# Kernel tuning notes

Hardware: AMD Instinct MI355X
Metric: run time of the kernel (lower is better)

Reference implementation:

```python
import jax, jax.numpy as jnp
import numpy as np

NUM_LAYERS = 2
D_MODEL = 64
D_INNER = 128   # expand * d_model
D_STATE = 128   # min(2*input_size, 256)
DT_RANK = 4     # ceil(d_model / 16)
D_CONV = 4
HIDDEN = 64


def _causal_dwconv(x, w, b):
    # x: [B, L, C], w: [C, K], b: [C]  -- causal depthwise conv (left pad K-1)
    K = w.shape[1]
    L = x.shape[1]
    xp = jnp.pad(x, ((0, 0), (K - 1, 0), (0, 0)))
    y = sum(xp[:, k:k + L, :] * w[:, k][None, None, :] for k in range(K))
    return y + b


def _selective_scan(u, delta, A, B, C, Dp):
    # u, delta: [b,L,d]; A: [d,n]; B, C: [b,L,n]; Dp: [d]
    dA = jnp.exp(jnp.einsum('bld,dn->lbdn', delta, A))          # [L,b,d,n]
    dBu = jnp.einsum('bld,bln,bld->lbdn', delta, B, u)           # [L,b,d,n]
    Ct = jnp.swapaxes(C, 0, 1)                                   # [L,b,n]

    def step(h, inp):
        dA_t, dBu_t, C_t = inp
        h = dA_t * h + dBu_t                                     # [b,d,n]
        y = jnp.einsum('bdn,bn->bd', h, C_t)
        return h, y

    h0 = jnp.zeros(dA.shape[1:], dA.dtype)
    _, ys = jax.lax.scan(step, h0, (dA, dBu, Ct))                # ys: [L,b,d]
    return jnp.swapaxes(ys, 0, 1) + u * Dp


def _mamba_layer(x, in_w, conv_w, conv_b, xproj_w, dt_w, dt_b, A_log, Dp, out_w):
    xz = x @ in_w.T                                              # [B,L,2*d_inner]
    xi, z = jnp.split(xz, 2, axis=-1)
    xi = jax.nn.silu(_causal_dwconv(xi, conv_w, conv_b))
    xdbl = xi @ xproj_w.T                                        # [B,L,dt_rank+2*d_state]
    delta = jax.nn.softplus(xdbl[..., :DT_RANK] @ dt_w.T + dt_b)
    Bm = xdbl[..., DT_RANK:DT_RANK + D_STATE]
    Cm = xdbl[..., DT_RANK + D_STATE:]
    A = -jnp.exp(A_log)
    y = _selective_scan(xi, delta, A, Bm, Cm, Dp)
    y = y * jax.nn.silu(z)
    return y @ out_w.T


def setup_inputs() -> dict:
    key = jax.random.key(0)
    ks = jax.random.split(key, 10)
    B, L = 4, 1024
    s = 0.05
    x = jax.random.normal(ks[0], (B, L, D_MODEL), dtype=jnp.float32)
    in_proj_w = jax.random.normal(ks[1], (NUM_LAYERS, 2 * D_INNER, D_MODEL)) * s
    conv_w = jax.random.normal(ks[2], (NUM_LAYERS, D_INNER, D_CONV)) * 0.2
    conv_b = jax.random.normal(ks[3], (NUM_LAYERS, D_INNER)) * 0.02
    x_proj_w = jax.random.normal(ks[4], (NUM_LAYERS, DT_RANK + 2 * D_STATE, D_INNER)) * s
    dt_w = jax.random.normal(ks[5], (NUM_LAYERS, D_INNER, DT_RANK)) * 0.1
    dt_b = jnp.full((NUM_LAYERS, D_INNER), -4.6, dtype=jnp.float32)  # softplus -> ~0.01
    # S4D-real init: A_log = log(1..d_state)
    A_log = jnp.log(jnp.broadcast_to(
        jnp.arange(1, D_STATE + 1, dtype=jnp.float32), (NUM_LAYERS, D_INNER, D_STATE)))
    D = jnp.ones((NUM_LAYERS, D_INNER), dtype=jnp.float32)
    out_proj_w = jax.random.normal(ks[6], (NUM_LAYERS, D_MODEL, D_INNER)) * s
    fc_w = jax.random.normal(ks[7], (HIDDEN, D_MODEL)) * s
    fc_b = jax.random.normal(ks[8], (HIDDEN,)) * 0.02
    return {"x": x, "in_proj_w": in_proj_w, "conv_w": conv_w, "conv_b": conv_b,
            "x_proj_w": x_proj_w, "dt_w": dt_w, "dt_b": dt_b, "A_log": A_log,
            "D": D, "out_proj_w": out_proj_w, "fc_w": fc_w, "fc_b": fc_b}


def reference(x, in_proj_w, conv_w, conv_b, x_proj_w, dt_w, dt_b, A_log, D, out_proj_w, fc_w, fc_b):
    h = x
    for l in range(NUM_LAYERS):
        h = _mamba_layer(h, in_proj_w[l], conv_w[l], conv_b[l], x_proj_w[l],
                         dt_w[l], dt_b[l], A_log[l], D[l], out_proj_w[l])
    return h @ fc_w.T + fc_b
```

## Files before the change

### kernel.cpp

```cpp
#include <hip/hip_runtime.h>
#include <hip/hip_bf16.h>

#define BB 4
#define LL 1024
#define DM 64
#define DI 128
#define DS 128
#define DTR 4
#define KC 4
#define RT 8
#define SGRP 8
#define L2E 1.44269504f

#define XWT_OFF   0
#define INWT_OFF  65536
#define OWT_OFF   98304
#define CWT_OFF   114688
#define CB_OFF    115712
#define DTWT_OFF  115968
#define DTB_OFF   116992
#define XWDT_OFF  117248

__device__ __forceinline__ float silu_f(float x) { return x / (1.f + __expf(-x)); }

__device__ __forceinline__ float ldf(const void* p, long i, unsigned bf) {
    return bf ? __bfloat162float(((const __hip_bfloat16*)p)[i]) : ((const float*)p)[i];
}

__device__ __forceinline__ void fma4(float4& acc, float s, const float4 w) {
    acc.x = fmaf(s, w.x, acc.x); acc.y = fmaf(s, w.y, acc.y);
    acc.z = fmaf(s, w.z, acc.z); acc.w = fmaf(s, w.w, acc.w);
}

__device__ __forceinline__ void probe_flags(const void* dtb, const void* fcw,
                                            unsigned& bfe, unsigned& bfw) {
    unsigned w = *(const unsigned*)dtb;
    bfe = (w == 0xC093C093u) ? 1u : 0u;
    const unsigned* p = (const unsigned*)fcw;
    int cnt = 0;
    for (int i = 0; i < 32; ++i) {
        unsigned m = p[i] & 0x7FFFu;
        if (m >= 0x3000u && m < 0x4200u) cnt++;
    }
    bfw = (cnt >= 28) ? 1u : 0u;
}

__global__ __launch_bounds__(256) void k_prep(
        const void* __restrict__ inw, const void* __restrict__ xw,
        const void* __restrict__ ow, const void* __restrict__ cw,
        const void* __restrict__ cb, const void* __restrict__ dtw,
        const void* __restrict__ dtb, const void* __restrict__ fcw,
        unsigned* __restrict__ flags, float* __restrict__ WT) {
    unsigned bfe, bfw;
    probe_flags(dtb, fcw, bfe, bfw);
    int bid = blockIdx.x, tid = threadIdx.x;
    if (bid < 28) {
        const void* src; long soff; int srcK; float* dst; int dstN; int n0, k0;
        if (bid < 16) {
            int l = bid >> 3, kt = (bid >> 2) & 1, nt = bid & 3;
            src = xw; srcK = 128; soff = (long)l * 260 * 128 + 4 * 128;
            n0 = nt * 64; k0 = kt * 64; dst = WT + XWT_OFF + l * 32768; dstN = 256;
        } else if (bid < 24) {
            int b2 = bid - 16, l = b2 >> 2, nt = b2 & 3;
            src = inw; srcK = 64; soff = (long)l * 256 * 64;
            n0 = nt * 64; k0 = 0; dst = WT + INWT_OFF + l * 16384; dstN = 256;
        } else {
            int b2 = bid - 24, l = b2 >> 1, kt = b2 & 1;
            src = ow; srcK = 128; soff = (long)l * 64 * 128;
            n0 = 0; k0 = kt * 64; dst = WT + OWT_OFF + l * 8192; dstN = 64;
        }
        __shared__ float tile[64 * 65];
        for (int i = tid; i < 4096; i += 256) {
            int ln = i >> 6, lk = i & 63;
            tile[ln * 65 + lk] = ldf(src, soff + (long)(n0 + ln) * srcK + k0 + lk, bfw);
        }
        __syncthreads();
        for (int i = tid; i < 4096; i += 256) {
            int lk = i >> 6, ln = i & 63;
            dst[(long)(k0 + lk) * dstN + n0 + ln] = tile[ln * 65 + lk];
        }
    } else {
        if (tid == 0) { flags[0] = bfe; flags[1] = bfw; flags[2] = bfe & bfw; }
        for (int j = tid; j < 1024; j += 256) {
            int l = j >> 9, t = (j >> 7) & 3, d = j & 127;
            WT[CWT_OFF + j] = ldf(cw, (long)l * 512 + d * 4 + t, bfw);
        }
        for (int j = tid; j < 256; j += 256) WT[CB_OFF + j] = ldf(cb, j, bfw);
        for (int j = tid; j < 1024; j += 256) {
            int l = j >> 9, r = (j >> 7) & 3, d = j & 127;
            WT[DTWT_OFF + j] = ldf(dtw, (long)l * 512 + d * 4 + r, bfw);
        }
        for (int j = tid; j < 256; j += 256) WT[DTB_OFF + j] = ldf(dtb, j, bfe);
        for (int j = tid; j < 1024; j += 256) {
            int l = j >> 9, rem = j & 511;
            WT[XWDT_OFF + j] = ldf(xw, (long)l * 260 * 128 + rem, bfw);
        }
    }
}

__global__ __launch_bounds__(256) void k_inproj(
        const void* __restrict__ xin, int xin_probe,
        const float* __restrict__ wt, const unsigned* __restrict__ flags,
        float* __restrict__ xzx, float* __restrict__ sz) {
    unsigned bfx = xin_probe ? flags[0] : 0u;
    int row0 = blockIdx.x * RT;
    int tid = threadIdx.x, lane = tid & 63, g = tid >> 6;
    __shared__ float act[RT * DM];
    for (int i = tid; i < RT * DM; i += 256)
        act[i] = ldf(xin, (long)(row0 + (i >> 6)) * DM + (i & 63), bfx);
    __syncthreads();
    const float4* wt4 = (const float4*)wt;
    float4 acc[2];
    acc[0] = make_float4(0.f, 0.f, 0.f, 0.f);
    acc[1] = make_float4(0.f, 0.f, 0.f, 0.f);
#pragma unroll 8
    for (int k4 = 0; k4 < DM / 4; ++k4) {
        float4 w0 = wt4[(k4 * 4 + 0) * 64 + lane];
        float4 w1 = wt4[(k4 * 4 + 1) * 64 + lane];
        float4 w2 = wt4[(k4 * 4 + 2) * 64 + lane];
        float4 w3 = wt4[(k4 * 4 + 3) * 64 + lane];
#pragma unroll
        for (int r = 0; r < 2; ++r) {
            float4 av = *(const float4*)&act[(g * 2 + r) * DM + k4 * 4];
            fma4(acc[r], av.x, w0); fma4(acc[r], av.y, w1);
            fma4(acc[r], av.z, w2); fma4(acc[r], av.w, w3);
        }
    }
    int n0 = lane * 4;
#pragma unroll
    for (int r = 0; r < 2; ++r) {
        int row = row0 + g * 2 + r;
        if (n0 < DI) {
            *(float4*)&xzx[(size_t)row * DI + n0] = acc[r];
        } else {
            float4 v;
            v.x = silu_f(acc[r].x); v.y = silu_f(acc[r].y);
            v.z = silu_f(acc[r].z); v.w = silu_f(acc[r].w);
            *(float4*)&sz[(size_t)row * DI + (n0 - DI)] = v;
        }
    }
}

__global__ __launch_bounds__(256) void k_xproj(
        const float* __restrict__ xzx,
        const float* __restrict__ cwT, const float* __restrict__ cbF,
        const float* __restrict__ xwT, const float* __restrict__ xwdtF,
        const float* __restrict__ dtwT, const float* __restrict__ dtbF,
        float* __restrict__ xiw, float* __restrict__ dlt,
        float* __restrict__ Bm, float* __restrict__ Cm) {
    int row0 = blockIdx.x * RT;
    int b = row0 >> 10, l0 = row0 & (LL - 1);
    int tid = threadIdx.x, lane = tid & 63, g = tid >> 6;
    __shared__ float xc[(RT + KC - 1) * DI];
    __shared__ float act[RT * DI];
    __shared__ float dtp[RT * DTR];
    for (int i = tid; i < (RT + KC - 1) * DI; i += 256) {
        int r = (i >> 7) - (KC - 1);
        int l = l0 + r;
        xc[i] = (l >= 0) ? xzx[((size_t)b * LL + l) * DI + (i & 127)] : 0.f;
    }
    __syncthreads();
    for (int i = tid; i < RT * DI; i += 256) {
        int r = i >> 7, d = i & 127;
        float a = cbF[d];
#pragma unroll
        for (int t = 0; t < KC; ++t) a = fmaf(xc[(r + t) * DI + d], cwT[t * DI + d], a);
        float v = silu_f(a);
        act[i] = v;
        xiw[(size_t)(row0 + r) * DI + d] = v;
    }
    __syncthreads();
    const float4* wt4 = (const float4*)xwT;
    float4 acc[2];
    acc[0] = make_float4(0.f, 0.f, 0.f, 0.f);
    acc[1] = make_float4(0.f, 0.f, 0.f, 0.f);
#pragma unroll 8
    for (int k4 = 0; k4 < DI / 4; ++k4) {
        float4 w0 = wt4[(k4 * 4 + 0) * 64 + lane];
        float4 w1 = wt4[(k4 * 4 + 1) * 64 + lane];
        float4 w2 = wt4[(k4 * 4 + 2) * 64 + lane];
        float4 w3 = wt4[(k4 * 4 + 3) * 64 + lane];
#pragma unroll
        for (int r = 0; r < 2; ++r) {
            float4 av = *(const float4*)&act[(g * 2 + r) * DI + k4 * 4];
            fma4(acc[r], av.x, w0); fma4(acc[r], av.y, w1);
            fma4(acc[r], av.z, w2); fma4(acc[r], av.w, w3);
        }
    }
    int n0 = lane * 4;
#pragma unroll
    for (int r = 0; r < 2; ++r) {
        int row = row0 + g * 2 + r;
        if (n0 < DS) *(float4*)&Bm[(size_t)row * DS + n0] = acc[r];
        else         *(float4*)&Cm[(size_t)row * DS + (n0 - DS)] = acc[r];
    }
    if (tid < RT * DTR) {
        int r = tid >> 2, i = tid & 3;
        float a = 0.f;
#pragma unroll
        for (int k4 = 0; k4 < DI / 4; ++k4) {
            float4 av = *(const float4*)&act[r * DI + k4 * 4];
            float4 wv = *(const float4*)&xwdtF[i * DI + k4 * 4];
            a = fmaf(av.x, wv.x, a); a = fmaf(av.y, wv.y, a);
            a = fmaf(av.z, wv.z, a); a = fmaf(av.w, wv.w, a);
        }
        dtp[tid] = a;
    }
    __syncthreads();
    if (tid < DI) {
        float dw0 = dtwT[0 * DI + tid], dw1 = dtwT[1 * DI + tid];
        float dw2 = dtwT[2 * DI + tid], dw3 = dtwT[3 * DI + tid];
        float bv = dtbF[tid];
#pragma unroll
        for (int r = 0; r < RT; ++r) {
            float a = bv;
            a = fmaf(dtp[r * 4 + 0], dw0, a);
            a = fmaf(dtp[r * 4 + 1], dw1, a);
            a = fmaf(dtp[r * 4 + 2], dw2, a);
            a = fmaf(dtp[r * 4 + 3], dw3, a);
            dlt[(size_t)(row0 + r) * DI + tid] = (a > 20.f) ? a : log1pf(__expf(a));
        }
    }
}

#define SCAN_GROUP(LI, BV, CV)                                              \
    {                                                                       \
        float dl0[SGRP], du0[SGRP], ea[SGRP], cv[SGRP];                     \
        _Pragma("unroll") for (int s = 0; s < SGRP; ++s) {                  \
            dl0[s] = dsh[d_loc][(LI) + s];                                  \
            du0[s] = dush[d_loc][(LI) + s];                                 \
        }                                                                   \
        _Pragma("unroll") for (int s = 0; s < SGRP; ++s)                    \
            ea[s] = exp2f(dl0[s] * A);                                      \
        _Pragma("unroll") for (int s = 0; s < SGRP; ++s) {                  \
            h = fmaf(ea[s], h, du0[s] * BV[s]);                             \
            cv[s] = h * CV[s];                                              \
        }                                                                   \
        _Pragma("unroll") for (int s = 0; s < SGRP; ++s)                    \
            Wl[s * 65 + t] = cv[s];                                         \
        float pt = 0.f;                                                     \
        _Pragma("unroll") for (int j = 0; j < 8; ++j) pt += Wl[rbase + j];  \
        pt += __shfl_xor(pt, 1, 64);                                        \
        pt += __shfl_xor(pt, 2, 64);                                        \
        pt += __shfl_xor(pt, 4, 64);                                        \
        if ((t & 7) == 0) ysh[((LI) + (t >> 3)) * 4 + w] = pt;              \
    }

__global__ __launch_bounds__(256) void k_scan(
        const float* __restrict__ dlt, const float* __restrict__ xiw,
        const float* __restrict__ Bm, const float* __restrict__ Cm,
        const void* __restrict__ Alog, long aoff,
        const unsigned* __restrict__ flags,
        float* __restrict__ y) {
    __shared__ float dsh[2][LL];
    __shared__ float dush[2][LL];
    __shared__ float ysh[LL * 4];
    __shared__ float Wred[4 * 520];
    int bid = blockIdx.x;
    int b = bid >> 6, dg = bid & 63;
    int tid = threadIdx.x, w = tid >> 6, t = tid & 63;
    int d_loc = w >> 1, half = w & 1;
    int d = dg * 2 + d_loc;
    int n = half * 64 + t;
    unsigned bfe = flags[0];
    float A = -L2E * __expf(ldf(Alog, aoff + (long)d * DS + n, bfe));
    for (int i = tid; i < 2 * LL; i += 256) {
        int l = i >> 1, dd = i & 1;
        size_t src = ((size_t)b * LL + l) * DI + dg * 2 + dd;
        float dl = dlt[src];
        dsh[dd][l] = dl;
        dush[dd][l] = dl * xiw[src];
    }
    __syncthreads();
    const float* Bg = Bm + (size_t)b * LL * DS + n;
    const float* Cg = Cm + (size_t)b * LL * DS + n;
    float* Wl = Wred + w * 520;
    int rbase = (t >> 3) * 65 + (t & 7) * 8;
    float h = 0.f;
    float B0[SGRP], C0[SGRP], B1[SGRP], C1[SGRP];
#pragma unroll
    for (int s = 0; s < SGRP; ++s) {
        B0[s] = Bg[(size_t)s * DS];
        C0[s] = Cg[(size_t)s * DS];
    }
    for (int li = 0; li < LL; li += 2 * SGRP) {
#pragma unroll
        for (int s = 0; s < SGRP; ++s) {
            B1[s] = Bg[(size_t)(li + SGRP + s) * DS];
            C1[s] = Cg[(size_t)(li + SGRP + s) * DS];
        }
        SCAN_GROUP(li, B0, C0);
#pragma unroll
        for (int s = 0; s < SGRP; ++s) {
            B0[s] = Bg[(size_t)(li + 2 * SGRP + s) * DS];
            C0[s] = Cg[(size_t)(li + 2 * SGRP + s) * DS];
        }
        SCAN_GROUP(li + SGRP, B1, C1);
    }
    __syncthreads();
    for (int i = tid; i < LL * 2; i += 256) {
        int l = i >> 1, dd = i & 1;
        y[((size_t)b * LL + l) * DI + dg * 2 + dd] =
            ysh[l * 4 + dd * 2] + ysh[l * 4 + dd * 2 + 1];
    }
}

__global__ __launch_bounds__(256) void k_out(
        const float* __restrict__ y, const float* __restrict__ sz,
        const float* __restrict__ xiw,
        const void* __restrict__ Dp, long doff,
        const unsigned* __restrict__ flags,
        const float* __restrict__ owT, float* __restrict__ hout) {
    unsigned bfe = flags[0];
    int row0 = blockIdx.x * RT;
    int tid = threadIdx.x, n = tid & 63, g = tid >> 6;
    __shared__ float act[RT * DI];
    __shared__ float Dsh[DI];
    if (tid < DI) Dsh[tid] = ldf(Dp, doff + tid, bfe);
    __syncthreads();
    for (int i = tid; i < RT * DI; i += 256) {
        size_t idx = (size_t)(row0 + (i >> 7)) * DI + (i & 127);
        act[i] = (y[idx] + xiw[idx] * Dsh[i & 127]) * sz[idx];
    }
    __syncthreads();
    float acc[2] = {0.f, 0.f};
#pragma unroll 8
    for (int k4 = 0; k4 < DI / 4; ++k4) {
        float w0 = owT[(k4 * 4 + 0) * DM + n];
        float w1 = owT[(k4 * 4 + 1) * DM + n];
        float w2 = owT[(k4 * 4 + 2) * DM + n];
        float w3 = owT[(k4 * 4 + 3) * DM + n];
#pragma unroll
        for (int r = 0; r < 2; ++r) {
            float4 av = *(const float4*)&act[(g * 2 + r) * DI + k4 * 4];
            acc[r] = fmaf(av.x, w0, acc[r]); acc[r] = fmaf(av.y, w1, acc[r]);
            acc[r] = fmaf(av.z, w2, acc[r]); acc[r] = fmaf(av.w, w3, acc[r]);
        }
    }
#pragma unroll
    for (int r = 0; r < 2; ++r)
        hout[(size_t)(row0 + g * 2 + r) * DM + n] = acc[r];
}

__global__ __launch_bounds__(256) void k_fc(
        const float* __restrict__ h, const void* __restrict__ fw,
        const void* __restrict__ fb, const unsigned* __restrict__ flags,
        void* __restrict__ out) {
    unsigned bfw = flags[1], obf = flags[2];
    int row0 = blockIdx.x * RT;
    int tid = threadIdx.x, n = tid & 63, g = tid >> 6;
    __shared__ float wsh[DM * 65];
    __shared__ float act[RT * DM];
    for (int i = tid; i < DM * DM; i += 256) {
        int nn = i >> 6, k = i & 63;
        wsh[k * 65 + nn] = ldf(fw, i, bfw);
    }
    for (int i = tid; i < RT * DM; i += 256)
        act[i] = h[(size_t)(row0 + (i >> 6)) * DM + (i & 63)];
    __syncthreads();
    float bv = ldf(fb, n, bfw);
    float acc[2] = {bv, bv};
#pragma unroll 8
    for (int k4 = 0; k4 < DM / 4; ++k4) {
        float w0 = wsh[(k4 * 4 + 0) * 65 + n];
        float w1 = wsh[(k4 * 4 + 1) * 65 + n];
        float w2 = wsh[(k4 * 4 + 2) * 65 + n];
        float w3 = wsh[(k4 * 4 + 3) * 65 + n];
#pragma unroll
        for (int r = 0; r < 2; ++r) {
            float4 av = *(const float4*)&act[(g * 2 + r) * DM + k4 * 4];
            acc[r] = fmaf(av.x, w0, acc[r]); acc[r] = fmaf(av.y, w1, acc[r]);
            acc[r] = fmaf(av.z, w2, acc[r]); acc[r] = fmaf(av.w, w3, acc[r]);
        }
    }
#pragma unroll
    for (int r = 0; r < 2; ++r) {
        size_t idx = (size_t)(row0 + g * 2 + r) * DM + n;
        if (obf) ((__hip_bfloat16*)out)[idx] = __float2bfloat16(acc[r]);
        else     ((float*)out)[idx] = acc[r];
    }
}

extern "C" void kernel_launch(void* const* d_in, const int* in_sizes, int n_in,
                              void* d_out, int out_size, void* d_ws, size_t ws_size,
                              hipStream_t stream) {
    const void* x    = d_in[0];
    const void* inw  = d_in[1];
    const void* cw   = d_in[2];
    const void* cb   = d_in[3];
    const void* xw   = d_in[4];
    const void* dtw  = d_in[5];
    const void* dtb  = d_in[6];
    const void* Alog = d_in[7];
    const void* Dp   = d_in[8];
    const void* ow   = d_in[9];
    const void* fcw  = d_in[10];
    const void* fcb  = d_in[11];

    const size_t NBL = (size_t)BB * LL;
    const int GB = (int)(NBL / RT);
    unsigned* flags = (unsigned*)d_ws;
    float* base = (float*)d_ws + 64;
    float* h1   = base;
    float* sz   = h1 + 262144;
    float* xiw  = sz + 524288;
    float* dlt  = xiw + 524288;
    float* Bmw  = dlt + 524288;
    float* Cmw  = Bmw + 524288;
    float* yw   = Cmw + 524288;
    float* xzx  = yw;
    float* WT   = (float*)d_out;

    k_prep<<<29, 256, 0, stream>>>(inw, xw, ow, cw, cb, dtw, dtb, fcw, flags, WT);

    for (int l = 0; l < 2; ++l) {
        const void* xin = (l == 0) ? x : (const void*)h1;
        int xmode = (l == 0) ? 1 : 0;
        k_inproj<<<GB, 256, 0, stream>>>(xin, xmode, WT + INWT_OFF + l * 16384, flags, xzx, sz);
        k_xproj<<<GB, 256, 0, stream>>>(xzx,
                                        WT + CWT_OFF + l * 512, WT + CB_OFF + l * 128,
                                        WT + XWT_OFF + l * 32768, WT + XWDT_OFF + l * 512,
                                        WT + DTWT_OFF + l * 512, WT + DTB_OFF + l * 128,
                                        xiw, dlt, Bmw, Cmw);
        long ao = (long)l * DI * DS;
        long dof = (long)l * DI;
        k_scan<<<BB * 64, 256, 0, stream>>>(dlt, xiw, Bmw, Cmw, Alog, ao, flags, yw);
        k_out<<<GB, 256, 0, stream>>>(yw, sz, xiw, Dp, dof, flags,
                                      WT + OWT_OFF + l * 8192, h1);
    }
    k_fc<<<GB, 256, 0, stream>>>(h1, fcw, fcb, flags, d_out);
}
```

Measured before the change: 317.4 us.

## Split selective scan into chunked local scans plus inter-chunk state correction

Replaces the single sequential scan over L=1024 per (batch, channel pair) with a chunked scan. First, a kernel scans 16 chunks of 64 steps independently from zero state and saves each chunk's end state and delta sum. Then a second kernel adds the contribution of the earlier chunks' states to each chunk's outputs, using the cumulative delta within the chunk. This gives far more blocks and a much shorter serial dependency chain. The cost is a second kernel, extra global traffic for the end states, and a correction loop that grows with chunk index; the D skip term also moves from the output kernel into the scan.

Result: faster. 292.1 us (-8.0%).

```diff
diff --git a/kernel.cpp b/kernel.cpp
--- a/kernel.cpp
+++ b/kernel.cpp
@@ -9,7 +9,11 @@
 #define DTR 4
 #define KC 4
 #define RT 8
-#define SGRP 8
+#define GRP 8
+#define CS 64
+#define NC 16
+#define SCD 8
+#define QL 32
 #define L2E 1.44269504f
 
 #define XWT_OFF   0
@@ -22,6 +26,7 @@
 #define XWDT_OFF  117248
 
 __device__ __forceinline__ float silu_f(float x) { return x / (1.f + __expf(-x)); }
+__device__ __forceinline__ float ex2(float x) { return __builtin_amdgcn_exp2f(x); }
 
 __device__ __forceinline__ float ldf(const void* p, long i, unsigned bf) {
     return bf ? __bfloat162float(((const __hip_bfloat16*)p)[i]) : ((const float*)p)[i];
@@ -223,104 +228,188 @@
     }
 }
 
-#define SCAN_GROUP(LI, BV, CV)                                              \
-    {                                                                       \
-        float dl0[SGRP], du0[SGRP], ea[SGRP], cv[SGRP];                     \
-        _Pragma("unroll") for (int s = 0; s < SGRP; ++s) {                  \
-            dl0[s] = dsh[d_loc][(LI) + s];                                  \
-            du0[s] = dush[d_loc][(LI) + s];                                 \
-        }                                                                   \
-        _Pragma("unroll") for (int s = 0; s < SGRP; ++s)                    \
-            ea[s] = exp2f(dl0[s] * A);                                      \
-        _Pragma("unroll") for (int s = 0; s < SGRP; ++s) {                  \
-            h = fmaf(ea[s], h, du0[s] * BV[s]);                             \
-            cv[s] = h * CV[s];                                              \
-        }                                                                   \
-        _Pragma("unroll") for (int s = 0; s < SGRP; ++s)                    \
-            Wl[s * 65 + t] = cv[s];                                         \
-        float pt = 0.f;                                                     \
-        _Pragma("unroll") for (int j = 0; j < 8; ++j) pt += Wl[rbase + j];  \
-        pt += __shfl_xor(pt, 1, 64);                                        \
-        pt += __shfl_xor(pt, 2, 64);                                        \
-        pt += __shfl_xor(pt, 4, 64);                                        \
-        if ((t & 7) == 0) ysh[((LI) + (t >> 3)) * 4 + w] = pt;              \
-    }
-
-__global__ __launch_bounds__(256) void k_scan(
+__global__ __launch_bounds__(512) void k_scan1(
         const float* __restrict__ dlt, const float* __restrict__ xiw,
         const float* __restrict__ Bm, const float* __restrict__ Cm,
         const void* __restrict__ Alog, long aoff,
+        const void* __restrict__ Dp, long doff,
         const unsigned* __restrict__ flags,
+        float* __restrict__ hend, float* __restrict__ S,
         float* __restrict__ y) {
-    __shared__ float dsh[2][LL];
-    __shared__ float dush[2][LL];
-    __shared__ float ysh[LL * 4];
-    __shared__ float Wred[4 * 520];
-    int bid = blockIdx.x;
-    int b = bid >> 6, dg = bid & 63;
+    __shared__ float Bsh[QL][DS];
+    __shared__ float Csh[QL][DS];
+    __shared__ float dsh[SCD][CS];
+    __shared__ float dush[SCD][CS];
+    __shared__ float ysh[CS][SCD];
+    __shared__ float Wred[SCD * 520];
+    int gid = blockIdx.x;
+    int dg = gid / (BB * NC);
+    int bc = gid % (BB * NC);
+    int b = bc / NC, c = bc % NC;
+    int d0 = dg * SCD;
     int tid = threadIdx.x, w = tid >> 6, t = tid & 63;
-    int d_loc = w >> 1, half = w & 1;
-    int d = dg * 2 + d_loc;
-    int n = half * 64 + t;
+    int d = d0 + w, c0 = c * CS;
     unsigned bfe = flags[0];
-    float A = -L2E * __expf(ldf(Alog, aoff + (long)d * DS + n, bfe));
-    for (int i = tid; i < 2 * LL; i += 256) {
-        int l = i >> 1, dd = i & 1;
-        size_t src = ((size_t)b * LL + l) * DI + dg * 2 + dd;
-        float dl = dlt[src];
-        dsh[dd][l] = dl;
-        dush[dd][l] = dl * xiw[src];
-    }
-    __syncthreads();
-    const float* Bg = Bm + (size_t)b * LL * DS + n;
-    const float* Cg = Cm + (size_t)b * LL * DS + n;
+    float A0 = -L2E * __expf(ldf(Alog, aoff + (long)d * DS + 2 * t, bfe));
+    float A1 = -L2E * __expf(ldf(Alog, aoff + (long)d * DS + 2 * t + 1, bfe));
+    {
+        size_t src = ((size_t)b * LL + c0 + t) * DI + d0 + w;
+        float dl = dlt[src], ul = xiw[src];
+        dsh[w][t] = dl;
+        dush[w][t] = dl * ul;
+        ysh[t][w] = ul * ldf(Dp, doff + d0 + w, bfe);
+    }
     float* Wl = Wred + w * 520;
     int rbase = (t >> 3) * 65 + (t & 7) * 8;
-    float h = 0.f;
-    float B0[SGRP], C0[SGRP], B1[SGRP], C1[SGRP];
-#pragma unroll
-    for (int s = 0; s < SGRP; ++s) {
-        B0[s] = Bg[(size_t)s * DS];
-        C0[s] = Cg[(size_t)s * DS];
-    }
-    for (int li = 0; li < LL; li += 2 * SGRP) {
-#pragma unroll
-        for (int s = 0; s < SGRP; ++s) {
-            B1[s] = Bg[(size_t)(li + SGRP + s) * DS];
-            C1[s] = Cg[(size_t)(li + SGRP + s) * DS];
-        }
-        SCAN_GROUP(li, B0, C0);
-#pragma unroll
-        for (int s = 0; s < SGRP; ++s) {
-            B0[s] = Bg[(size_t)(li + 2 * SGRP + s) * DS];
-            C0[s] = Cg[(size_t)(li + 2 * SGRP + s) * DS];
-        }
-        SCAN_GROUP(li + SGRP, B1, C1);
-    }
-    __syncthreads();
-    for (int i = tid; i < LL * 2; i += 256) {
-        int l = i >> 1, dd = i & 1;
-        y[((size_t)b * LL + l) * DI + dg * 2 + dd] =
-            ysh[l * 4 + dd * 2] + ysh[l * 4 + dd * 2 + 1];
+    float h0 = 0.f, h1v = 0.f, sumd = 0.f;
+    for (int hh = 0; hh < 2; ++hh) {
+        __syncthreads();
+        for (int i = tid; i < QL * 32; i += 512) {
+            int r = i >> 5, c4 = (i & 31) * 4;
+            size_t g = ((size_t)b * LL + c0 + hh * QL + r) * DS + c4;
+            *(float4*)&Bsh[r][c4] = *(const float4*)&Bm[g];
+            *(float4*)&Csh[r][c4] = *(const float4*)&Cm[g];
+        }
+        __syncthreads();
+        for (int li = 0; li < QL; li += GRP) {
+            int lg = hh * QL + li;
+            float dl[GRP], du[GRP], ea0[GRP], ea1[GRP], cv[GRP];
+            float2 Bv[GRP], Cv[GRP];
+#pragma unroll
+            for (int s = 0; s < GRP; ++s) {
+                dl[s] = dsh[w][lg + s];
+                du[s] = dush[w][lg + s];
+                Bv[s] = ((const float2*)Bsh[li + s])[t];
+                Cv[s] = ((const float2*)Csh[li + s])[t];
+            }
+#pragma unroll
+            for (int s = 0; s < GRP; ++s) {
+                ea0[s] = ex2(dl[s] * A0);
+                ea1[s] = ex2(dl[s] * A1);
+                sumd += dl[s];
+            }
+#pragma unroll
+            for (int s = 0; s < GRP; ++s) {
+                h0  = fmaf(ea0[s], h0,  du[s] * Bv[s].x);
+                h1v = fmaf(ea1[s], h1v, du[s] * Bv[s].y);
+                cv[s] = fmaf(h0, Cv[s].x, h1v * Cv[s].y);
+            }
+#pragma unroll
+            for (int s = 0; s < GRP; ++s) Wl[s * 65 + t] = cv[s];
+            float pt = 0.f;
+#pragma unroll
+            for (int j = 0; j < 8; ++j) pt += Wl[rbase + j];
+            pt += __shfl_xor(pt, 1, 64);
+            pt += __shfl_xor(pt, 2, 64);
+            pt += __shfl_xor(pt, 4, 64);
+            if ((t & 7) == 0) ysh[lg + (t >> 3)][w] += pt;
+        }
+    }
+    if (c < NC - 1) {
+        size_t hbase = (((size_t)b * DI + d) * NC + c) * DS;
+        ((float2*)(hend + hbase))[t] = make_float2(h0, h1v);
+        if (t == 0) S[((size_t)b * DI + d) * NC + c] = sumd;
+    }
+    __syncthreads();
+    for (int i = tid; i < CS * SCD; i += 512) {
+        int l = i >> 3, dd = i & 7;
+        y[((size_t)b * LL + c0 + l) * DI + d0 + dd] = ysh[l][dd];
+    }
+}
+
+__global__ __launch_bounds__(512) void k_scan2(
+        const float* __restrict__ dlt, const float* __restrict__ Cm,
+        const void* __restrict__ Alog, long aoff,
+        const unsigned* __restrict__ flags,
+        const float* __restrict__ hend, const float* __restrict__ S,
+        float* __restrict__ y) {
+    __shared__ float Csh[QL][DS];
+    __shared__ float cdsh[SCD][CS];
+    __shared__ float ysh[CS][SCD];
+    __shared__ float Wred[SCD * 520];
+    int gid = blockIdx.x;
+    int dg = gid / (BB * (NC - 1));
+    int bc = gid % (BB * (NC - 1));
+    int b = bc / (NC - 1), c = bc % (NC - 1) + 1;
+    int d0 = dg * SCD;
+    int tid = threadIdx.x, w = tid >> 6, t = tid & 63;
+    int d = d0 + w, c0 = c * CS;
+    unsigned bfe = flags[0];
+    float A0 = -L2E * __expf(ldf(Alog, aoff + (long)d * DS + 2 * t, bfe));
+    float A1 = -L2E * __expf(ldf(Alog, aoff + (long)d * DS + 2 * t + 1, bfe));
+    {
+        float a = dlt[((size_t)b * LL + c0 + t) * DI + d0 + w];
+#pragma unroll
+        for (int off = 1; off < 64; off <<= 1) {
+            float nn = __shfl(a, t - off, 64);
+            if (t >= off) a += nn;
+        }
+        cdsh[w][t] = a;
+    }
+    float hi0 = 0.f, hi1 = 0.f, ssum = 0.f;
+    const float2* hep = (const float2*)(hend + (((size_t)b * DI + d) * NC) * DS);
+    const float* Sp = S + ((size_t)b * DI + d) * NC;
+    for (int cc = c - 1; cc >= 0; --cc) {
+        float2 he = hep[(size_t)cc * (DS / 2) + t];
+        hi0 = fmaf(ex2(A0 * ssum), he.x, hi0);
+        hi1 = fmaf(ex2(A1 * ssum), he.y, hi1);
+        ssum += Sp[cc];
+    }
+    float* Wl = Wred + w * 520;
+    int rbase = (t >> 3) * 65 + (t & 7) * 8;
+    for (int hh = 0; hh < 2; ++hh) {
+        __syncthreads();
+        for (int i = tid; i < QL * 32; i += 512) {
+            int r = i >> 5, c4 = (i & 31) * 4;
+            *(float4*)&Csh[r][c4] =
+                *(const float4*)&Cm[((size_t)b * LL + c0 + hh * QL + r) * DS + c4];
+        }
+        __syncthreads();
+        for (int li = 0; li < QL; li += GRP) {
+            int lg = hh * QL + li;
+            float cd[GRP], ea0[GRP], ea1[GRP], cv[GRP];
+            float2 Cv[GRP];
+#pragma unroll
+            for (int s = 0; s < GRP; ++s) {
+                cd[s] = cdsh[w][lg + s];
+                Cv[s] = ((const float2*)Csh[li + s])[t];
+            }
+#pragma unroll
+            for (int s = 0; s < GRP; ++s) {
+                ea0[s] = ex2(cd[s] * A0);
+                ea1[s] = ex2(cd[s] * A1);
+            }
+#pragma unroll
+            for (int s = 0; s < GRP; ++s)
+                cv[s] = fmaf(hi0 * ea0[s], Cv[s].x, hi1 * ea1[s] * Cv[s].y);
+#pragma unroll
+            for (int s = 0; s < GRP; ++s) Wl[s * 65 + t] = cv[s];
+            float pt = 0.f;
+#pragma unroll
+            for (int j = 0; j < 8; ++j) pt += Wl[rbase + j];
+            pt += __shfl_xor(pt, 1, 64);
+            pt += __shfl_xor(pt, 2, 64);
+            pt += __shfl_xor(pt, 4, 64);
+            if ((t & 7) == 0) ysh[lg + (t >> 3)][w] = pt;
+        }
+    }
+    __syncthreads();
+    for (int i = tid; i < CS * SCD; i += 512) {
+        int l = i >> 3, dd = i & 7;
+        size_t idx = ((size_t)b * LL + c0 + l) * DI + d0 + dd;
+        y[idx] += ysh[l][dd];
     }
 }
 
 __global__ __launch_bounds__(256) void k_out(
         const float* __restrict__ y, const float* __restrict__ sz,
-        const float* __restrict__ xiw,
-        const void* __restrict__ Dp, long doff,
-        const unsigned* __restrict__ flags,
         const float* __restrict__ owT, float* __restrict__ hout) {
-    unsigned bfe = flags[0];
     int row0 = blockIdx.x * RT;
     int tid = threadIdx.x, n = tid & 63, g = tid >> 6;
     __shared__ float act[RT * DI];
-    __shared__ float Dsh[DI];
-    if (tid < DI) Dsh[tid] = ldf(Dp, doff + tid, bfe);
-    __syncthreads();
     for (int i = tid; i < RT * DI; i += 256) {
         size_t idx = (size_t)(row0 + (i >> 7)) * DI + (i & 127);
-        act[i] = (y[idx] + xiw[idx] * Dsh[i & 127]) * sz[idx];
+        act[i] = y[idx] * sz[idx];
     }
     __syncthreads();
     float acc[2] = {0.f, 0.f};
@@ -408,6 +497,8 @@
     float* Bmw  = dlt + 524288;
     float* Cmw  = Bmw + 524288;
     float* yw   = Cmw + 524288;
+    float* hend = yw + 524288;
+    float* S    = hend + 1048576;
     float* xzx  = yw;
     float* WT   = (float*)d_out;
 
@@ -424,9 +515,11 @@
                                         xiw, dlt, Bmw, Cmw);
         long ao = (long)l * DI * DS;
         long dof = (long)l * DI;
-        k_scan<<<BB * 64, 256, 0, stream>>>(dlt, xiw, Bmw, Cmw, Alog, ao, flags, yw);
-        k_out<<<GB, 256, 0, stream>>>(yw, sz, xiw, Dp, dof, flags,
-                                      WT + OWT_OFF + l * 8192, h1);
+        k_scan1<<<(DI / SCD) * BB * NC, 512, 0, stream>>>(
+            dlt, xiw, Bmw, Cmw, Alog, ao, Dp, dof, flags, hend, S, yw);
+        k_scan2<<<(DI / SCD) * BB * (NC - 1), 512, 0, stream>>>(
+            dlt, Cmw, Alog, ao, flags, hend, S, yw);
+        k_out<<<GB, 256, 0, stream>>>(yw, sz, WT + OWT_OFF + l * 8192, h1);
     }
     k_fc<<<GB, 256, 0, stream>>>(h1, fcw, fcb, flags, d_out);
 }
```
